# Performance work log

Hardware: AMD Instinct MI355X
Metric: run time of the kernel (lower is better)

The kernel has to match this reference:

```python
import jax, jax.numpy as jnp
import numpy as np

D_MODEL = 2048
N_HEADS = 8
N_KV = 4
HEAD_DIM = 256
WINDOW = 1024
EPS = 1e-6
ROPE_BASE = 10000.0


def _rms_norm(x, w):
    # x: [..., D]; matches torch: x * rsqrt(mean(x^2) + eps) * w
    return x * jax.lax.rsqrt(jnp.mean(x * x, axis=-1, keepdims=True) + EPS) * w


def _rope_cos_sin(pos):
    # pos: [T] ints -> cos/sin: [T, HEAD_DIM] (cat(freqs, freqs) as in source)
    inv_freq = 1.0 / (ROPE_BASE ** (jnp.arange(0, HEAD_DIM, 2, dtype=jnp.float32) / HEAD_DIM))
    freqs = pos.astype(jnp.float32)[:, None] * inv_freq[None, :]  # [T, D/2]
    emb = jnp.concatenate([freqs, freqs], axis=-1)                # [T, D]
    return jnp.cos(emb), jnp.sin(emb)


def _apply_rotary(x, cos, sin):
    # x: [B, H, T, D]; interleaved rotate-half exactly as the torch code
    x1 = x[..., 0::2]
    x2 = x[..., 1::2]
    x_rot = jnp.stack([-x2, x1], axis=-1).reshape(x.shape)
    return x * cos[None, None, :, :] + x_rot * sin[None, None, :, :]


def setup_inputs() -> dict:
    key = jax.random.key(0)
    ks = jax.random.split(key, 8)
    B, T = 1, 4096
    s = 0.02
    return {
        "x": jax.random.normal(ks[0], (B, T, D_MODEL), dtype=jnp.float32),
        "pos": jnp.arange(T, dtype=jnp.int32),
        "Wq": jax.random.normal(ks[1], (N_HEADS * HEAD_DIM, D_MODEL), dtype=jnp.float32) * s,
        "Wk": jax.random.normal(ks[2], (N_KV * HEAD_DIM, D_MODEL), dtype=jnp.float32) * s,
        "Wv": jax.random.normal(ks[3], (N_KV * HEAD_DIM, D_MODEL), dtype=jnp.float32) * s,
        "Wo": jax.random.normal(ks[4], (D_MODEL, N_HEADS * HEAD_DIM), dtype=jnp.float32) * s,
        "q_norm_w": jnp.ones((HEAD_DIM,), dtype=jnp.float32),
        "k_norm_w": jnp.ones((HEAD_DIM,), dtype=jnp.float32),
    }


def reference(x, pos, Wq, Wk, Wv, Wo, q_norm_w, k_norm_w):
    B, T, _ = x.shape
    # projections (torch Linear: y = x @ W.T)
    q = (x @ Wq.T).reshape(B, T, N_HEADS, HEAD_DIM).transpose(0, 2, 1, 3)  # [B,H,T,D]
    k = (x @ Wk.T).reshape(B, T, N_KV, HEAD_DIM).transpose(0, 2, 1, 3)    # [B,Hkv,T,D]
    v = (x @ Wv.T).reshape(B, T, N_KV, HEAD_DIM).transpose(0, 2, 1, 3)
    # per-head RMSNorm
    q = _rms_norm(q, q_norm_w)
    k = _rms_norm(k, k_norm_w)
    # RoPE
    cos, sin = _rope_cos_sin(pos)
    q = _apply_rotary(q, cos, sin)
    k = _apply_rotary(k, cos, sin)
    # GQA repeat: [B,Hkv,T,D] -> [B,H,T,D]
    rep = N_HEADS // N_KV
    k = jnp.repeat(k, rep, axis=1)
    v = jnp.repeat(v, rep, axis=1)
    # full scores + sliding-window causal mask (faithful to source)
    scores = jnp.einsum("bhqd,bhkd->bhqk", q, k) / jnp.sqrt(jnp.float32(HEAD_DIM))
    i = jnp.arange(T)[:, None]
    j = jnp.arange(T)[None, :]
    allowed = (j <= i) & (j >= i - WINDOW + 1)  # [T,T]
    scores = jnp.where(allowed[None, None, :, :], scores, -jnp.inf)
    attn = jax.nn.softmax(scores, axis=-1)
    y = jnp.einsum("bhqk,bhkd->bhqd", attn, v)
    y = y.transpose(0, 2, 1, 3).reshape(B, T, N_HEADS * HEAD_DIM)
    return y @ Wo.T
```

## Files before the change

kernel.cpp:

```cpp
#include <hip/hip_runtime.h>
#include <cstdint>
#include <cmath>

typedef __bf16 bf16x8 __attribute__((ext_vector_type(8)));
typedef float  f32x4  __attribute__((ext_vector_type(4)));

#define DEVI __device__ __forceinline__

#define SEQ 4096
#define NH 8
#define NKV 4
#define HD 256
#define WIN 1024

DEVI void gload16(const void* g, void* l) {
  __builtin_amdgcn_global_load_lds((const __attribute__((address_space(1))) void*)g,
                                   (__attribute__((address_space(3))) void*)l,
                                   16, 0, 0);
}

DEVI bf16x8 ld8f(const float* p) {
  const f32x4 a = *(const f32x4*)p;
  const f32x4 b = *(const f32x4*)(p + 4);
  bf16x8 r;
#pragma unroll
  for (int j = 0; j < 4; ++j) { r[j] = (__bf16)a[j]; r[4 + j] = (__bf16)b[j]; }
  return r;
}

DEVI void st1(float* p, float v)  { *p = v; }
DEVI void st1(__bf16* p, float v) { *p = (__bf16)v; }

__global__ __launch_bounds__(256)
void cvt_all(const float* __restrict__ x,  const float* __restrict__ wq,
             const float* __restrict__ wk, const float* __restrict__ wv,
             const float* __restrict__ wo,
             __bf16* __restrict__ xb, __bf16* __restrict__ wqkvb,
             __bf16* __restrict__ wob) {
  const size_t g = (size_t)blockIdx.x * 256 + threadIdx.x;
  const float* src; __bf16* dst; size_t off;
  if      (g < 1048576) { src = x;  dst = xb;               off = g; }
  else if (g < 1572864) { src = wq; dst = wqkvb;            off = g - 1048576; }
  else if (g < 1835008) { src = wk; dst = wqkvb + 4194304;  off = g - 1572864; }
  else if (g < 2097152) { src = wv; dst = wqkvb + 6291456;  off = g - 1835008; }
  else                  { src = wo; dst = wob;              off = g - 2097152; }
  *(bf16x8*)(dst + off * 8) = ld8f(src + off * 8);
}

template <typename TC>
__global__ __launch_bounds__(256, 2)
void gemm_bt(const __bf16* __restrict__ A, const __bf16* __restrict__ B,
             TC* __restrict__ C, int N, int K) {
  __shared__ __bf16 As2[2][128][32];
  __shared__ __bf16 Bs2[2][128][32];
  const int tid  = threadIdx.x;
  const int lane = tid & 63;
  const int wave = tid >> 6;
  const int l15  = lane & 15;
  const int l4   = lane >> 4;

  const int lin  = blockIdx.x + gridDim.x * blockIdx.y;
  const int xcd  = lin & 7;
  const int kk   = lin >> 3;
  const int row0 = (xcd * 4 + (kk & 3)) * 128;
  const int col0 = (kk >> 2) * 128;

  const int wm   = (wave >> 1) * 64;
  const int wn   = (wave & 1) * 64;

  f32x4 acc[4][4] = {};

  for (int k0 = 0; k0 < K; k0 += 64) {
    __syncthreads();
#pragma unroll
    for (int i = 0; i < 4; ++i) {
      const int s  = i * 256 + tid;
      const int ch = s >> 9, r = (s >> 2) & 127, c4 = s & 3;
      gload16(A + (size_t)(row0 + r) * K + k0 + ch * 32 + c4 * 8,
              (char*)As2 + (i * 256 + wave * 64) * 16);
    }
#pragma unroll
    for (int i = 0; i < 4; ++i) {
      const int s  = i * 256 + tid;
      const int ch = s >> 9, r = (s >> 2) & 127, c4 = s & 3;
      gload16(B + (size_t)(col0 + r) * K + k0 + ch * 32 + c4 * 8,
              (char*)Bs2 + (i * 256 + wave * 64) * 16);
    }
    __syncthreads();
#pragma unroll
    for (int ch = 0; ch < 2; ++ch) {
      bf16x8 af[4], bfr[4];
#pragma unroll
      for (int i = 0; i < 4; ++i)
        af[i] = *(const bf16x8*)&As2[ch][wm + i * 16 + l15][l4 * 8];
#pragma unroll
      for (int i = 0; i < 4; ++i)
        bfr[i] = *(const bf16x8*)&Bs2[ch][wn + i * 16 + l15][l4 * 8];
#pragma unroll
      for (int i = 0; i < 4; ++i)
#pragma unroll
        for (int j = 0; j < 4; ++j)
          acc[i][j] = __builtin_amdgcn_mfma_f32_16x16x32_bf16(af[i], bfr[j], acc[i][j], 0, 0, 0);
    }
  }

#pragma unroll
  for (int i = 0; i < 4; ++i) {
#pragma unroll
    for (int reg = 0; reg < 4; ++reg) {
      const int row = row0 + wm + i * 16 + l4 * 4 + reg;
      TC* crow = C + (size_t)row * N + col0 + wn + l15;
#pragma unroll
      for (int j = 0; j < 4; ++j)
        st1(crow + j * 16, acc[i][j][reg]);
    }
  }
}

__global__ __launch_bounds__(256)
void norm_rope_tv(__bf16* __restrict__ qkv, __bf16* __restrict__ Vt,
                  const float* __restrict__ qw, const float* __restrict__ kw,
                  const int* __restrict__ pos) {
  if (blockIdx.x < 12288) {
    const int gw   = blockIdx.x * 4 + (threadIdx.x >> 6);
    const int lane = threadIdx.x & 63;
    __bf16* base; const float* w; int t;
    if (gw < SEQ * NH) {
      t = gw >> 3;
      base = qkv + (size_t)t * 4096 + (gw & 7) * HD;
      w = qw;
    } else {
      const int g = gw - SEQ * NH;
      t = g >> 2;
      base = qkv + (size_t)t * 4096 + 2048 + (g & 3) * HD;
      w = kw;
    }

    const int d0 = lane * 4;
    float v[4]; float ss = 0.f;
#pragma unroll
    for (int j = 0; j < 4; ++j) { v[j] = (float)base[d0 + j]; ss += v[j] * v[j]; }
#pragma unroll
    for (int off = 1; off < 64; off <<= 1) ss += __shfl_xor(ss, off);
    const float rms = rsqrtf(ss * (1.0f / 256.0f) + 1e-6f);
    const float p = (float)pos[t];

    float n[4];
#pragma unroll
    for (int j = 0; j < 4; ++j) n[j] = v[j] * rms * w[d0 + j];

    float outv[4];
#pragma unroll
    for (int e = 0; e < 4; e += 2) {
      const int i0 = d0 + e, i1 = i0 + 1;
      const float f0 = exp2f(-(float)(i0 & 127) * 0.103810253f);
      const float f1 = exp2f(-(float)(i1 & 127) * 0.103810253f);
      float s0, cc0, s1, cc1;
      sincosf(p * f0, &s0, &cc0);
      sincosf(p * f1, &s1, &cc1);
      outv[e]     = n[e] * cc0 - n[e + 1] * s0;
      outv[e + 1] = n[e + 1] * cc1 + n[e] * s1;
    }
#pragma unroll
    for (int j = 0; j < 4; ++j) base[d0 + j] = (__bf16)outv[j];
  } else {
    __shared__ __bf16 tile[64][72];
    const int b   = blockIdx.x - 12288;
    const int tid = threadIdx.x;
    const int tb  = (b & 63) * 64;
    const int yy  = b >> 6;
    const int kvh = yy >> 2;
    const int db  = (yy & 3) * 64;
#pragma unroll
    for (int i = 0; i < 2; ++i) {
      const int s = i * 256 + tid;
      const int r = s >> 3, c = (s & 7) * 8;
      bf16x8 val = *(const bf16x8*)(qkv + (size_t)(tb + r) * 4096 + 3072 + kvh * HD + db + c);
#pragma unroll
      for (int j = 0; j < 8; ++j) tile[r][c + j] = val[j];
    }
    __syncthreads();
#pragma unroll
    for (int i = 0; i < 2; ++i) {
      const int s = i * 256 + tid;
      const int r = s >> 3, c = (s & 7) * 8;
      bf16x8 outv;
#pragma unroll
      for (int j = 0; j < 8; ++j) outv[j] = tile[c + j][r];
      *(bf16x8*)(Vt + (size_t)(kvh * HD + db + r) * SEQ + tb + c) = outv;
    }
  }
}

__global__ __launch_bounds__(256, 2)
void attn_fwd(const __bf16* __restrict__ qkv, const __bf16* __restrict__ Vt,
              __bf16* __restrict__ Y) {
  __shared__ __bf16 Ks2[8][64][32];
  __shared__ __bf16 Vts2[2][256][32];
  __shared__ __bf16 Ps[4][16][72];
  const int tid  = threadIdx.x;
  const int lane = tid & 63;
  const int wave = tid >> 6;
  const int l15  = lane & 15;
  const int l4   = lane >> 4;
  const int q0   = blockIdx.x * 64;
  const int head = blockIdx.y;
  const int kvh  = head >> 1;
  const int qw   = q0 + wave * 16;

  bf16x8 qf[8];
  const __bf16* qrow = qkv + (size_t)(qw + l15) * 4096 + head * HD;
#pragma unroll
  for (int ks = 0; ks < 8; ++ks) {
    bf16x8 t = *(const bf16x8*)(qrow + ks * 32 + l4 * 8);
#pragma unroll
    for (int j = 0; j < 8; ++j) t[j] = (__bf16)((float)t[j] * 0.0625f);
    qf[ks] = t;
  }

  f32x4 o[16] = {};
  float l_run[4] = {0.f, 0.f, 0.f, 0.f};

  int lo = q0 - (WIN - 1); if (lo < 0) lo = 0;
  const int kt0 = lo >> 6;
  const int kt1 = (q0 + 63) >> 6;

  for (int kt = kt0; kt <= kt1; ++kt) {
    const int kb = kt * 64;
    __syncthreads();
#pragma unroll
    for (int i = 0; i < 8; ++i) {
      const int s = i * 256 + tid;
      gload16(qkv + (size_t)(kb + ((s >> 2) & 63)) * 4096 + 2048 + kvh * HD
                  + (s >> 8) * 32 + (s & 3) * 8,
              (char*)Ks2 + (i * 256 + wave * 64) * 16);
    }
#pragma unroll
    for (int i = 0; i < 8; ++i) {
      const int s = i * 256 + tid;
      gload16(Vt + ((size_t)kvh * HD + ((s >> 2) & 255)) * SEQ + kb
                 + (s >> 10) * 32 + (s & 3) * 8,
              (char*)Vts2 + (i * 256 + wave * 64) * 16);
    }
    __syncthreads();

    f32x4 s_acc[4] = {};
#pragma unroll
    for (int kn = 0; kn < 4; ++kn) {
#pragma unroll
      for (int ks = 0; ks < 8; ++ks) {
        bf16x8 kf = *(const bf16x8*)&Ks2[ks][kn * 16 + l15][l4 * 8];
        s_acc[kn] = __builtin_amdgcn_mfma_f32_16x16x32_bf16(qf[ks], kf, s_acc[kn], 0, 0, 0);
      }
    }

#pragma unroll
    for (int reg = 0; reg < 4; ++reg) {
      const int r  = l4 * 4 + reg;
      const int qg = qw + r;
      float ps = 0.f;
#pragma unroll
      for (int kn = 0; kn < 4; ++kn) {
        const int kg = kb + kn * 16 + l15;
        const bool ok = (kg <= qg) && (kg > qg - WIN);
        const float p = ok ? __expf(fminf(s_acc[kn][reg], 34.f) - 34.f) : 0.f;
        ps += p;
        Ps[wave][r][kn * 16 + l15] = (__bf16)p;
      }
      l_run[reg] += ps;
    }

#pragma unroll
    for (int ks2 = 0; ks2 < 2; ++ks2) {
      bf16x8 pf = *(const bf16x8*)&Ps[wave][l15][ks2 * 32 + l4 * 8];
#pragma unroll
      for (int dn = 0; dn < 16; ++dn) {
        bf16x8 vf = *(const bf16x8*)&Vts2[ks2][dn * 16 + l15][l4 * 8];
        o[dn] = __builtin_amdgcn_mfma_f32_16x16x32_bf16(pf, vf, o[dn], 0, 0, 0);
      }
    }
  }

#pragma unroll
  for (int reg = 0; reg < 4; ++reg) {
#pragma unroll
    for (int off = 1; off < 16; off <<= 1)
      l_run[reg] += __shfl_xor(l_run[reg], off);
    const float inv = 1.0f / l_run[reg];
    const int q = qw + l4 * 4 + reg;
    __bf16* yrow = Y + ((size_t)q * NH + head) * HD + l15;
#pragma unroll
    for (int dn = 0; dn < 16; ++dn)
      yrow[dn * 16] = (__bf16)(o[dn][reg] * inv);
  }
}

extern "C" void kernel_launch(void* const* d_in, const int* in_sizes, int n_in,
                              void* d_out, int out_size, void* d_ws, size_t ws_size,
                              hipStream_t stream) {
  (void)in_sizes; (void)n_in; (void)out_size; (void)ws_size;
  const float* x   = (const float*)d_in[0];
  const int*   pos = (const int*)d_in[1];
  const float* Wq  = (const float*)d_in[2];
  const float* Wk  = (const float*)d_in[3];
  const float* Wv  = (const float*)d_in[4];
  const float* Wo  = (const float*)d_in[5];
  const float* qw  = (const float*)d_in[6];
  const float* kw  = (const float*)d_in[7];
  float* out = (float*)d_out;

  char* ws = (char*)d_ws;
  const size_t MB = 1024 * 1024;
  __bf16* qkv_ws = (__bf16*)(ws);
  __bf16* vt_ws  = (__bf16*)(ws + 32 * MB);
  __bf16* y_ws   = (__bf16*)(ws + 40 * MB);
  __bf16* xb     = (__bf16*)(ws + 56 * MB);
  __bf16* wqkvb  = (__bf16*)(ws + 72 * MB);
  __bf16* wob    = (__bf16*)(ws + 88 * MB);

  cvt_all<<<dim3(10240), dim3(256), 0, stream>>>(x, Wq, Wk, Wv, Wo, xb, wqkvb, wob);
  gemm_bt<__bf16><<<dim3(32, 32), dim3(256), 0, stream>>>(xb, wqkvb, qkv_ws, 4096, 2048);
  norm_rope_tv<<<dim3(13312), dim3(256), 0, stream>>>(qkv_ws, vt_ws, qw, kw, pos);
  attn_fwd<<<dim3(64, 8), dim3(256), 0, stream>>>(qkv_ws, vt_ws, y_ws);
  gemm_bt<float><<<dim3(32, 16), dim3(256), 0, stream>>>(y_ws, wob, out, 2048, 2048);
}
```

Baseline: 321.6 us.

## Fuse V transpose into QKV GEMM epilogue and skip masking on fully visible tiles

The QKV GEMM epilogue now writes the V columns directly in transposed layout, which removes the separate transpose blocks from the norm/rope kernel. The conversion and norm/rope kernels each process four items per thread with smaller grids. Attention skips the per-element window mask check when a whole key tile is visible. The transposed store writes 8-byte chunks strided by SEQ, which may coalesce less well than the old LDS transpose.

```diff
diff --git a/kernel.cpp b/kernel.cpp
--- a/kernel.cpp
+++ b/kernel.cpp
@@ -3,6 +3,7 @@
 #include <cmath>
 
 typedef __bf16 bf16x8 __attribute__((ext_vector_type(8)));
+typedef __bf16 bf16x4 __attribute__((ext_vector_type(4)));
 typedef float  f32x4  __attribute__((ext_vector_type(4)));
 
 #define DEVI __device__ __forceinline__
@@ -37,20 +38,23 @@
              const float* __restrict__ wo,
              __bf16* __restrict__ xb, __bf16* __restrict__ wqkvb,
              __bf16* __restrict__ wob) {
-  const size_t g = (size_t)blockIdx.x * 256 + threadIdx.x;
-  const float* src; __bf16* dst; size_t off;
-  if      (g < 1048576) { src = x;  dst = xb;               off = g; }
-  else if (g < 1572864) { src = wq; dst = wqkvb;            off = g - 1048576; }
-  else if (g < 1835008) { src = wk; dst = wqkvb + 4194304;  off = g - 1572864; }
-  else if (g < 2097152) { src = wv; dst = wqkvb + 6291456;  off = g - 1835008; }
-  else                  { src = wo; dst = wob;              off = g - 2097152; }
-  *(bf16x8*)(dst + off * 8) = ld8f(src + off * 8);
+#pragma unroll
+  for (int k = 0; k < 4; ++k) {
+    const size_t g = (size_t)blockIdx.x * 256 + threadIdx.x + (size_t)k * 655360;
+    const float* src; __bf16* dst; size_t off;
+    if      (g < 1048576) { src = x;  dst = xb;               off = g; }
+    else if (g < 1572864) { src = wq; dst = wqkvb;            off = g - 1048576; }
+    else if (g < 1835008) { src = wk; dst = wqkvb + 4194304;  off = g - 1572864; }
+    else if (g < 2097152) { src = wv; dst = wqkvb + 6291456;  off = g - 1835008; }
+    else                  { src = wo; dst = wob;              off = g - 2097152; }
+    *(bf16x8*)(dst + off * 8) = ld8f(src + off * 8);
+  }
 }
 
 template <typename TC>
 __global__ __launch_bounds__(256, 2)
 void gemm_bt(const __bf16* __restrict__ A, const __bf16* __restrict__ B,
-             TC* __restrict__ C, int N, int K) {
+             TC* __restrict__ C, __bf16* __restrict__ vt, int N, int K) {
   __shared__ __bf16 As2[2][128][32];
   __shared__ __bf16 Bs2[2][128][32];
   const int tid  = threadIdx.x;
@@ -104,26 +108,44 @@
     }
   }
 
-#pragma unroll
-  for (int i = 0; i < 4; ++i) {
-#pragma unroll
-    for (int reg = 0; reg < 4; ++reg) {
-      const int row = row0 + wm + i * 16 + l4 * 4 + reg;
-      TC* crow = C + (size_t)row * N + col0 + wn + l15;
-#pragma unroll
-      for (int j = 0; j < 4; ++j)
-        st1(crow + j * 16, acc[i][j][reg]);
+  if (vt != nullptr && col0 >= 3072) {
+#pragma unroll
+    for (int i = 0; i < 4; ++i) {
+      const int t0 = row0 + wm + i * 16 + l4 * 4;
+#pragma unroll
+      for (int j = 0; j < 4; ++j) {
+        const int nv = col0 - 3072 + wn + l15 + j * 16;
+        bf16x4 v;
+#pragma unroll
+        for (int reg = 0; reg < 4; ++reg) v[reg] = (__bf16)acc[i][j][reg];
+        *(bf16x4*)(vt + (size_t)nv * SEQ + t0) = v;
+      }
+    }
+  } else {
+#pragma unroll
+    for (int i = 0; i < 4; ++i) {
+#pragma unroll
+      for (int reg = 0; reg < 4; ++reg) {
+        const int row = row0 + wm + i * 16 + l4 * 4 + reg;
+        TC* crow = C + (size_t)row * N + col0 + wn + l15;
+#pragma unroll
+        for (int j = 0; j < 4; ++j)
+          st1(crow + j * 16, acc[i][j][reg]);
+      }
     }
   }
 }
 
 __global__ __launch_bounds__(256)
-void norm_rope_tv(__bf16* __restrict__ qkv, __bf16* __restrict__ Vt,
-                  const float* __restrict__ qw, const float* __restrict__ kw,
-                  const int* __restrict__ pos) {
-  if (blockIdx.x < 12288) {
-    const int gw   = blockIdx.x * 4 + (threadIdx.x >> 6);
-    const int lane = threadIdx.x & 63;
+void norm_rope(__bf16* __restrict__ qkv,
+               const float* __restrict__ qw, const float* __restrict__ kw,
+               const int* __restrict__ pos) {
+  const int lane = threadIdx.x & 63;
+  const int wave = threadIdx.x >> 6;
+  const int d0   = lane * 4;
+#pragma unroll
+  for (int ri = 0; ri < 4; ++ri) {
+    const int gw = blockIdx.x * 16 + wave * 4 + ri;
     __bf16* base; const float* w; int t;
     if (gw < SEQ * NH) {
       t = gw >> 3;
@@ -136,7 +158,6 @@
       w = kw;
     }
 
-    const int d0 = lane * 4;
     float v[4]; float ss = 0.f;
 #pragma unroll
     for (int j = 0; j < 4; ++j) { v[j] = (float)base[d0 + j]; ss += v[j] * v[j]; }
@@ -163,32 +184,6 @@
     }
 #pragma unroll
     for (int j = 0; j < 4; ++j) base[d0 + j] = (__bf16)outv[j];
-  } else {
-    __shared__ __bf16 tile[64][72];
-    const int b   = blockIdx.x - 12288;
-    const int tid = threadIdx.x;
-    const int tb  = (b & 63) * 64;
-    const int yy  = b >> 6;
-    const int kvh = yy >> 2;
-    const int db  = (yy & 3) * 64;
-#pragma unroll
-    for (int i = 0; i < 2; ++i) {
-      const int s = i * 256 + tid;
-      const int r = s >> 3, c = (s & 7) * 8;
-      bf16x8 val = *(const bf16x8*)(qkv + (size_t)(tb + r) * 4096 + 3072 + kvh * HD + db + c);
-#pragma unroll
-      for (int j = 0; j < 8; ++j) tile[r][c + j] = val[j];
-    }
-    __syncthreads();
-#pragma unroll
-    for (int i = 0; i < 2; ++i) {
-      const int s = i * 256 + tid;
-      const int r = s >> 3, c = (s & 7) * 8;
-      bf16x8 outv;
-#pragma unroll
-      for (int j = 0; j < 8; ++j) outv[j] = tile[c + j][r];
-      *(bf16x8*)(Vt + (size_t)(kvh * HD + db + r) * SEQ + tb + c) = outv;
-    }
   }
 }
 
@@ -254,20 +249,36 @@
       }
     }
 
-#pragma unroll
-    for (int reg = 0; reg < 4; ++reg) {
-      const int r  = l4 * 4 + reg;
-      const int qg = qw + r;
-      float ps = 0.f;
-#pragma unroll
-      for (int kn = 0; kn < 4; ++kn) {
-        const int kg = kb + kn * 16 + l15;
-        const bool ok = (kg <= qg) && (kg > qg - WIN);
-        const float p = ok ? __expf(fminf(s_acc[kn][reg], 34.f) - 34.f) : 0.f;
-        ps += p;
-        Ps[wave][r][kn * 16 + l15] = (__bf16)p;
-      }
-      l_run[reg] += ps;
+    const bool allvis = (kb + 63 <= qw) && (kb >= qw - 1008);
+    if (allvis) {
+#pragma unroll
+      for (int reg = 0; reg < 4; ++reg) {
+        const int r = l4 * 4 + reg;
+        float ps = 0.f;
+#pragma unroll
+        for (int kn = 0; kn < 4; ++kn) {
+          const float p = __expf(fminf(s_acc[kn][reg], 34.f) - 34.f);
+          ps += p;
+          Ps[wave][r][kn * 16 + l15] = (__bf16)p;
+        }
+        l_run[reg] += ps;
+      }
+    } else {
+#pragma unroll
+      for (int reg = 0; reg < 4; ++reg) {
+        const int r  = l4 * 4 + reg;
+        const int qg = qw + r;
+        float ps = 0.f;
+#pragma unroll
+        for (int kn = 0; kn < 4; ++kn) {
+          const int kg = kb + kn * 16 + l15;
+          const bool ok = (kg <= qg) && (kg > qg - WIN);
+          const float p = ok ? __expf(fminf(s_acc[kn][reg], 34.f) - 34.f) : 0.f;
+          ps += p;
+          Ps[wave][r][kn * 16 + l15] = (__bf16)p;
+        }
+        l_run[reg] += ps;
+      }
     }
 
 #pragma unroll
@@ -318,9 +329,9 @@
   __bf16* wqkvb  = (__bf16*)(ws + 72 * MB);
   __bf16* wob    = (__bf16*)(ws + 88 * MB);
 
-  cvt_all<<<dim3(10240), dim3(256), 0, stream>>>(x, Wq, Wk, Wv, Wo, xb, wqkvb, wob);
-  gemm_bt<__bf16><<<dim3(32, 32), dim3(256), 0, stream>>>(xb, wqkvb, qkv_ws, 4096, 2048);
-  norm_rope_tv<<<dim3(13312), dim3(256), 0, stream>>>(qkv_ws, vt_ws, qw, kw, pos);
+  cvt_all<<<dim3(2560), dim3(256), 0, stream>>>(x, Wq, Wk, Wv, Wo, xb, wqkvb, wob);
+  gemm_bt<__bf16><<<dim3(32, 32), dim3(256), 0, stream>>>(xb, wqkvb, qkv_ws, vt_ws, 4096, 2048);
+  norm_rope<<<dim3(3072), dim3(256), 0, stream>>>(qkv_ws, qw, kw, pos);
   attn_fwd<<<dim3(64, 8), dim3(256), 0, stream>>>(qkv_ws, vt_ws, y_ws);
-  gemm_bt<float><<<dim3(32, 16), dim3(256), 0, stream>>>(y_ws, wob, out, 2048, 2048);
-}
+  gemm_bt<float><<<dim3(32, 16), dim3(256), 0, stream>>>(y_ws, wob, out, (__bf16*)nullptr, 2048, 2048);
+}
```

New measurement: 325.3 us. No clear change (+1.2%).
